# Kernel tuning notes

Hardware: AMD Instinct MI355X
Metric: run time of the kernel (lower is better)

Reference implementation:

```python
import jax, jax.numpy as jnp
import numpy as np

D_MODEL = 1024
NUM_HEADS = 16
HEAD_DIM = D_MODEL // NUM_HEADS


def setup_inputs() -> dict:
    key = jax.random.key(0)
    ks = jax.random.split(key, 9)
    s = D_MODEL ** -0.5  # roughly like nn.Linear init scale
    x = jax.random.normal(ks[0], (4, 2048, D_MODEL), dtype=jnp.float32)
    Wq = jax.random.normal(ks[1], (D_MODEL, D_MODEL), dtype=jnp.float32) * s
    bq = jax.random.normal(ks[2], (D_MODEL,), dtype=jnp.float32) * s
    Wk = jax.random.normal(ks[3], (D_MODEL, D_MODEL), dtype=jnp.float32) * s
    bk = jax.random.normal(ks[4], (D_MODEL,), dtype=jnp.float32) * s
    Wv = jax.random.normal(ks[5], (D_MODEL, D_MODEL), dtype=jnp.float32) * s
    bv = jax.random.normal(ks[6], (D_MODEL,), dtype=jnp.float32) * s
    Wo = jax.random.normal(ks[7], (D_MODEL, D_MODEL), dtype=jnp.float32) * s
    bo = jax.random.normal(ks[8], (D_MODEL,), dtype=jnp.float32) * s
    return {"x": x, "Wq": Wq, "bq": bq, "Wk": Wk, "bk": bk,
            "Wv": Wv, "bv": bv, "Wo": Wo, "bo": bo}


def reference(x, Wq, bq, Wk, bk, Wv, bv, Wo, bo):
    B, S, D = x.shape
    H, Dh = NUM_HEADS, HEAD_DIM
    scale = Dh ** -0.5
    # nn.Linear: x @ W.T + b
    q = (x @ Wq.T + bq).reshape(B, S, H, Dh)
    k = (x @ Wk.T + bk).reshape(B, S, H, Dh)
    v = (x @ Wv.T + bv).reshape(B, S, H, Dh)
    # scores: (B, H, S, S), full materialization as in the original bmm path
    dp = scale * jnp.einsum('bqhd,bkhd->bhqk', q, k)
    att = jax.nn.softmax(dp, axis=-1)
    out = jnp.einsum('bhqk,bkhd->bqhd', att, v).reshape(B, S, D)
    return out @ Wo.T + bo
```

## Files before the change

kernel.cpp:

```cpp
#include <hip/hip_runtime.h>
#include <stdint.h>

typedef __attribute__((ext_vector_type(8))) __bf16 bf16x8;
typedef __attribute__((ext_vector_type(4))) float floatx4;

#define DEV __device__ __forceinline__

DEV unsigned short f2bf(float f) {
    union { float f; unsigned u; } uf; uf.f = f;
    unsigned u = uf.u;
    unsigned r = (u + 0x7fffu + ((u >> 16) & 1u)) >> 16;
    return (unsigned short)r;
}

DEV float fast_exp2(float x) {
#if __has_builtin(__builtin_amdgcn_exp2f)
    return __builtin_amdgcn_exp2f(x);
#else
    return exp2f(x);
#endif
}

DEV unsigned pack_trunc2(float lo, float hi) {
    return __builtin_amdgcn_perm(__float_as_uint(hi), __float_as_uint(lo), 0x07060302u);
}

DEV void async16(const void* g, void* l) {
    __builtin_amdgcn_global_load_lds(
        (const __attribute__((address_space(1))) void*)g,
        (__attribute__((address_space(3))) void*)l, 16, 0, 0);
}

__global__ void cast_all_kernel(const float* __restrict__ x,
                                const float* __restrict__ Wq, const float* __restrict__ Wk,
                                const float* __restrict__ Wv, const float* __restrict__ Wo,
                                const float* __restrict__ bq, const float* __restrict__ bk,
                                const float* __restrict__ bv,
                                unsigned short* __restrict__ xb,
                                unsigned short* __restrict__ wqkv,
                                unsigned short* __restrict__ wo,
                                float* __restrict__ bqkv) {
    const int NX = 2097152;
    const int NW = 262144;
    int i = blockIdx.x * blockDim.x + threadIdx.x;
    if (i < NX) {
        float4 v = reinterpret_cast<const float4*>(x)[i];
        ushort4 o;
        o.x = f2bf(v.x); o.y = f2bf(v.y); o.z = f2bf(v.z); o.w = f2bf(v.w);
        reinterpret_cast<ushort4*>(xb)[i] = o;
        return;
    }
    int j = i - NX;
    if (j < 4 * NW) {
        int seg = j >> 18, off = j & (NW - 1);
        const float* src = (seg == 0) ? Wq : (seg == 1) ? Wk : (seg == 2) ? Wv : Wo;
        unsigned short* dst = (seg < 3) ? (wqkv + seg * 1048576) : wo;
        float4 v = reinterpret_cast<const float4*>(src)[off];
        ushort4 o;
        o.x = f2bf(v.x); o.y = f2bf(v.y); o.z = f2bf(v.z); o.w = f2bf(v.w);
        reinterpret_cast<ushort4*>(dst)[off] = o;
        return;
    }
    int k = j - 4 * NW;
    if (k < 768) {
        int seg = k >> 8, off = k & 255;
        const float* src = (seg == 0) ? bq : (seg == 1) ? bk : bv;
        reinterpret_cast<float4*>(bqkv)[k] = reinterpret_cast<const float4*>(src)[off];
    }
}

template <int MODE>
__global__ __launch_bounds__(256)
void gemm128(const unsigned short* __restrict__ A,
             const unsigned short* __restrict__ B,
             const float* __restrict__ bias,
             unsigned short* __restrict__ q_ws,
             unsigned short* __restrict__ k_ws,
             unsigned short* __restrict__ v_ws,
             float* __restrict__ fout) {
    constexpr int K = 1024;
    __shared__ alignas(16) unsigned short smem[128 * 136];
    unsigned short* sA = smem;
    unsigned short* sB = smem + 128 * 64;
    unsigned short* sT = smem;
    float* sT32 = reinterpret_cast<float*>(smem);

    const int tid = threadIdx.x;
    const int w = tid >> 6, lane = tid & 63, quad = lane >> 4, l16 = lane & 15;
    const int wr = w >> 1, wc = w & 1;
    const int bm = blockIdx.x, bn = blockIdx.y;
    const int arow0 = bm * 128, brow0 = bn * 128;

    floatx4 acc[4][4];
#pragma unroll
    for (int i = 0; i < 4; i++)
#pragma unroll
        for (int j = 0; j < 4; j++) acc[i][j] = (floatx4){0.f, 0.f, 0.f, 0.f};

    for (int k0 = 0; k0 < K; k0 += 64) {
#pragma unroll
        for (int i = 0; i < 4; i++) {
            int cb = i * 256 + w * 64;
            int ci = cb + lane;
            int row = ci >> 3, cl = ci & 7, cs = cl ^ (row & 7);
            async16(A + (size_t)(arow0 + row) * K + k0 + cs * 8, (char*)sA + cb * 16);
            async16(B + (size_t)(brow0 + row) * K + k0 + cs * 8, (char*)sB + cb * 16);
        }
        __syncthreads();
#pragma unroll
        for (int kk = 0; kk < 2; kk++) {
            bf16x8 aF[4], bF[4];
#pragma unroll
            for (int i = 0; i < 4; i++) {
                int row = wr * 64 + i * 16 + l16;
                int c = kk * 4 + quad, ph = c ^ (row & 7);
                aF[i] = *reinterpret_cast<const bf16x8*>(sA + row * 64 + ph * 8);
            }
#pragma unroll
            for (int j = 0; j < 4; j++) {
                int row = wc * 64 + j * 16 + l16;
                int c = kk * 4 + quad, ph = c ^ (row & 7);
                bF[j] = *reinterpret_cast<const bf16x8*>(sB + row * 64 + ph * 8);
            }
#pragma unroll
            for (int i = 0; i < 4; i++)
#pragma unroll
                for (int j = 0; j < 4; j++)
                    acc[i][j] = __builtin_amdgcn_mfma_f32_16x16x32_bf16(
                        aF[i], bF[j], acc[i][j], 0, 0, 0);
        }
        __syncthreads();
    }

    if (MODE == 1) {
#pragma unroll
        for (int ch = 0; ch < 2; ch++) {
            if (ch) __syncthreads();
            if (wr == ch) {
#pragma unroll
                for (int j = 0; j < 4; j++) {
                    const int c = wc * 64 + j * 16 + l16;
                    const float bia = bias[brow0 + c];
#pragma unroll
                    for (int i = 0; i < 4; i++) {
                        int s_loc = i * 16 + quad * 4;
#pragma unroll
                        for (int r = 0; r < 4; r++)
                            sT32[(s_loc + r) * 132 + c] = acc[i][j][r] + bia;
                    }
                }
            }
            __syncthreads();
            const int cpos = (tid & 31) * 4;
#pragma unroll
            for (int it = 0; it < 8; it++) {
                int s_loc = (tid >> 5) + it * 8;
                int grow = arow0 + ch * 64 + s_loc;
                float4 vv = *reinterpret_cast<const float4*>(sT32 + s_loc * 132 + cpos);
                *reinterpret_cast<float4*>(fout + (size_t)grow * 1024 + brow0 + cpos) = vv;
            }
        }
    } else if (bn < 16) {
        unsigned short* dst = (bn < 8) ? q_ws : k_ws;
        const float sc = (bn < 8) ? 0.18033688f : 1.0f;
#pragma unroll
        for (int j = 0; j < 4; j++) {
            const int c = wc * 64 + j * 16 + l16;
            const float bia = bias[brow0 + c];
#pragma unroll
            for (int i = 0; i < 4; i++) {
                int s_loc = wr * 64 + i * 16 + quad * 4;
#pragma unroll
                for (int r = 0; r < 4; r++)
                    sT[(s_loc + r) * 136 + c] = f2bf((acc[i][j][r] + bia) * sc);
            }
        }
        __syncthreads();
        const int nnbase = (bn & 7) * 128;
        const int c0 = (tid & 15) * 8;
        const int h = (nnbase + c0) >> 6, d = c0 & 63;
#pragma unroll
        for (int it = 0; it < 8; it++) {
            int s_loc = (tid >> 4) + it * 16;
            int s = arow0 + s_loc;
            int bb = s >> 11, s4 = s & 2047;
            uint4 vdat = *reinterpret_cast<const uint4*>(sT + s_loc * 136 + c0);
            *reinterpret_cast<uint4*>(
                dst + ((size_t)(bb * 16 + h) * 2048 + s4) * 64 + d) = vdat;
        }
    } else {
#pragma unroll
        for (int j = 0; j < 4; j++) {
            const int c = wc * 64 + j * 16 + l16;
            const float bia = bias[brow0 + c];
#pragma unroll
            for (int i = 0; i < 4; i++) {
#pragma unroll
                for (int r = 0; r < 4; r++) {
                    int v = wr * 64 + (quad * 4 + r) * 4 + i;
                    sT[c * 136 + v] = f2bf(acc[i][j][r] + bia);
                }
            }
        }
        __syncthreads();
        const int bb = bm >> 4, blk = bm & 15;
        const int chunk = tid & 15;
#pragma unroll
        for (int it = 0; it < 8; it++) {
            int row = (tid >> 4) + it * 16;
            int h = (bn - 16) * 2 + (row >> 6), d = row & 63;
            ushort4 lo = *reinterpret_cast<const ushort4*>(sT + row * 136 + chunk * 8);
            ushort4 hi = *reinterpret_cast<const ushort4*>(sT + row * 136 + chunk * 8 + 4);
            size_t off = ((size_t)(bb * 16 + h) * 64 + d) * 2048 + blk * 128 + chunk * 8;
            *reinterpret_cast<ushort4*>(v_ws + off) = lo;
            *reinterpret_cast<ushort4*>(v_ws + off + 4) = hi;
        }
    }
}

__global__ __launch_bounds__(256, 4)
void attn_kernel(const unsigned short* __restrict__ q_ws,
                 const unsigned short* __restrict__ k_ws,
                 const unsigned short* __restrict__ v_ws,
                 unsigned short* __restrict__ o_ws) {
    __shared__ alignas(16) unsigned short smem[20480];

    const int tid = threadIdx.x;
    const int w = tid >> 6, lane = tid & 63, quad = lane >> 4, l16 = lane & 15;
    const int id = blockIdx.x;
    const int bh = (id >> 7) * 8 + (id & 7);
    const int q0 = ((id >> 3) & 15) * 128;
    const size_t base = (size_t)bh * 2048 * 64;

    unsigned short* sPw = smem + 16384 + w * 1024;

    bf16x8 aQ[2][2];
#pragma unroll
    for (int g = 0; g < 2; g++) {
        int qrow = q0 + g * 64 + w * 16 + l16;
        const unsigned short* qp = q_ws + base + (size_t)qrow * 64 + quad * 8;
        aQ[g][0] = *reinterpret_cast<const bf16x8*>(qp);
        aQ[g][1] = *reinterpret_cast<const bf16x8*>(qp + 32);
    }

    const unsigned short* kg[2];
    const unsigned short* vg[2];
    int loff[2];
#pragma unroll
    for (int it = 0; it < 2; it++) {
        int ci = it * 256 + tid;
        int row = ci >> 3, cl = ci & 7, cs = cl ^ (row & 7);
        kg[it] = k_ws + base + (size_t)row * 64 + cs * 8;
        vg[it] = v_ws + base + (size_t)row * 2048 + cs * 8;
        loff[it] = ci * 8;
    }

    const __bf16 one = (__bf16)1.0f;
    const bf16x8 vOnes = {one, one, one, one, one, one, one, one};

    floatx4 oAcc[2][4], rsAcc[2];
#pragma unroll
    for (int g = 0; g < 2; g++) {
#pragma unroll
        for (int j = 0; j < 4; j++) oAcc[g][j] = (floatx4){0.f, 0.f, 0.f, 0.f};
        rsAcc[g] = (floatx4){0.f, 0.f, 0.f, 0.f};
    }

    {
#pragma unroll
        for (int it = 0; it < 2; it++) {
            async16(kg[it], smem + loff[it]);
            async16(vg[it], smem + 8192 + loff[it]);
        }
    }

    for (int t = 0; t < 32; t++) {
        const int b = t & 1;
        const unsigned short* sK = smem + b * 4096;
        const unsigned short* sVt = smem + 8192 + b * 4096;
        __syncthreads();

        if (t < 31) {
            const int kv0 = (t + 1) * 64;
            unsigned short* dK = smem + (b ^ 1) * 4096;
            unsigned short* dV = smem + 8192 + (b ^ 1) * 4096;
#pragma unroll
            for (int it = 0; it < 2; it++) {
                async16(kg[it] + (size_t)kv0 * 64, dK + loff[it]);
                async16(vg[it] + kv0, dV + loff[it]);
            }
        }

#pragma unroll
        for (int g = 0; g < 2; g++) {
            floatx4 sAcc[4];
#pragma unroll
            for (int j = 0; j < 4; j++) sAcc[j] = (floatx4){0.f, 0.f, 0.f, 0.f};
#pragma unroll
            for (int kk = 0; kk < 2; kk++) {
#pragma unroll
                for (int j = 0; j < 4; j++) {
                    int krow = j * 16 + l16;
                    int ph = (kk * 4 + quad) ^ (krow & 7);
                    bf16x8 aK = *reinterpret_cast<const bf16x8*>(sK + krow * 64 + ph * 8);
                    sAcc[j] = __builtin_amdgcn_mfma_f32_16x16x32_bf16(
                        aK, aQ[g][kk], sAcc[j], 0, 0, 0);
                }
            }

            {
                float e00 = fast_exp2(sAcc[0][0]), e10 = fast_exp2(sAcc[1][0]);
                float e20 = fast_exp2(sAcc[2][0]), e30 = fast_exp2(sAcc[3][0]);
                float e01 = fast_exp2(sAcc[0][1]), e11 = fast_exp2(sAcc[1][1]);
                float e21 = fast_exp2(sAcc[2][1]), e31 = fast_exp2(sAcc[3][1]);
                float e02 = fast_exp2(sAcc[0][2]), e12 = fast_exp2(sAcc[1][2]);
                float e22 = fast_exp2(sAcc[2][2]), e32 = fast_exp2(sAcc[3][2]);
                float e03 = fast_exp2(sAcc[0][3]), e13 = fast_exp2(sAcc[1][3]);
                float e23 = fast_exp2(sAcc[2][3]), e33 = fast_exp2(sAcc[3][3]);
                uint4 w0, w1;
                w0.x = pack_trunc2(e00, e10);
                w0.y = pack_trunc2(e20, e30);
                w0.z = pack_trunc2(e01, e11);
                w0.w = pack_trunc2(e21, e31);
                w1.x = pack_trunc2(e02, e12);
                w1.y = pack_trunc2(e22, e32);
                w1.z = pack_trunc2(e03, e13);
                w1.w = pack_trunc2(e23, e33);
                const int xr = l16 & 7;
                *reinterpret_cast<uint4*>(sPw + l16 * 64 + (((2 * quad) ^ xr) << 3)) = w0;
                *reinterpret_cast<uint4*>(sPw + l16 * 64 + (((2 * quad + 1) ^ xr) << 3)) = w1;
            }
            asm volatile("s_waitcnt lgkmcnt(0)" ::: "memory");
            __builtin_amdgcn_sched_barrier(0);

            bf16x8 aP[2];
#pragma unroll
            for (int ks = 0; ks < 2; ks++)
                aP[ks] = *reinterpret_cast<const bf16x8*>(
                    sPw + l16 * 64 + (((ks * 4 + quad) ^ (l16 & 7)) << 3));
#pragma unroll
            for (int jd = 0; jd < 4; jd++) {
                int drow = jd * 16 + l16;
#pragma unroll
                for (int ks = 0; ks < 2; ks++) {
                    int ph = (ks * 4 + quad) ^ (drow & 7);
                    bf16x8 bV = *reinterpret_cast<const bf16x8*>(sVt + drow * 64 + ph * 8);
                    oAcc[g][jd] = __builtin_amdgcn_mfma_f32_16x16x32_bf16(
                        aP[ks], bV, oAcc[g][jd], 0, 0, 0);
                }
            }
#pragma unroll
            for (int ks = 0; ks < 2; ks++)
                rsAcc[g] = __builtin_amdgcn_mfma_f32_16x16x32_bf16(
                    aP[ks], vOnes, rsAcc[g], 0, 0, 0);
        }
    }

    const int bb = bh >> 4, h = bh & 15;
#pragma unroll
    for (int g = 0; g < 2; g++) {
        float inv[4];
#pragma unroll
        for (int r = 0; r < 4; r++) inv[r] = 1.0f / rsAcc[g][r];
#pragma unroll
        for (int jd = 0; jd < 4; jd++) {
            int d = jd * 16 + l16;
#pragma unroll
            for (int r = 0; r < 4; r++) {
                int s = q0 + g * 64 + w * 16 + quad * 4 + r;
                float v = oAcc[g][jd][r] * inv[r];
                o_ws[((size_t)bb * 2048 + s) * 1024 + h * 64 + d] = f2bf(v);
            }
        }
    }
}

extern "C" void kernel_launch(void* const* d_in, const int* in_sizes, int n_in,
                              void* d_out, int out_size, void* d_ws, size_t ws_size,
                              hipStream_t stream) {
    const float* x  = (const float*)d_in[0];
    const float* Wq = (const float*)d_in[1];
    const float* bq = (const float*)d_in[2];
    const float* Wk = (const float*)d_in[3];
    const float* bk = (const float*)d_in[4];
    const float* Wv = (const float*)d_in[5];
    const float* bv = (const float*)d_in[6];
    const float* Wo = (const float*)d_in[7];
    const float* bo = (const float*)d_in[8];
    float* out = (float*)d_out;

    char* ws = (char*)d_ws;
    unsigned short* xb   = (unsigned short*)(ws);
    unsigned short* wqkv = (unsigned short*)(ws + (16ull << 20));
    unsigned short* wo   = (unsigned short*)(ws + (22ull << 20));
    float*          bqkv = (float*)(ws + (24ull << 20));
    unsigned short* q_ws = (unsigned short*)(ws + (25ull << 20));
    unsigned short* k_ws = (unsigned short*)(ws + (41ull << 20));
    unsigned short* v_ws = (unsigned short*)(ws + (57ull << 20));
    unsigned short* o_ws = xb;

    cast_all_kernel<<<12291, 256, 0, stream>>>(x, Wq, Wk, Wv, Wo, bq, bk, bv,
                                               xb, wqkv, wo, bqkv);

    gemm128<0><<<dim3(64, 24), 256, 0, stream>>>(xb, wqkv, bqkv, q_ws, k_ws, v_ws, nullptr);
    attn_kernel<<<1024, 256, 0, stream>>>(q_ws, k_ws, v_ws, o_ws);
    gemm128<1><<<dim3(64, 8), 256, 0, stream>>>(o_ws, wo, bo, nullptr, nullptr, nullptr, out);
}
```

Measured before the change: 275.9 us.

## Interleave two query groups in attention loop and retile output projection GEMM

The attention inner loop now computes QK^T for both 64-row query groups together, sharing each K fragment load between the two groups. The exp2 and pack of the second group are interleaved with the PV MFMAs of the first, so MFMA and VALU work can overlap. Separately, the output projection moves to a dedicated 128x64-tile GEMM launched on a 64x16 grid, doubling block count to fill more CUs. The cost is higher register pressure from holding two score sets, plus more A-tile reloads in the projection.

```diff
diff --git a/kernel.cpp b/kernel.cpp
--- a/kernel.cpp
+++ b/kernel.cpp
@@ -83,7 +83,6 @@
     unsigned short* sA = smem;
     unsigned short* sB = smem + 128 * 64;
     unsigned short* sT = smem;
-    float* sT32 = reinterpret_cast<float*>(smem);
 
     const int tid = threadIdx.x;
     const int w = tid >> 6, lane = tid & 63, quad = lane >> 4, l16 = lane & 15;
@@ -132,35 +131,7 @@
         __syncthreads();
     }
 
-    if (MODE == 1) {
-#pragma unroll
-        for (int ch = 0; ch < 2; ch++) {
-            if (ch) __syncthreads();
-            if (wr == ch) {
-#pragma unroll
-                for (int j = 0; j < 4; j++) {
-                    const int c = wc * 64 + j * 16 + l16;
-                    const float bia = bias[brow0 + c];
-#pragma unroll
-                    for (int i = 0; i < 4; i++) {
-                        int s_loc = i * 16 + quad * 4;
-#pragma unroll
-                        for (int r = 0; r < 4; r++)
-                            sT32[(s_loc + r) * 132 + c] = acc[i][j][r] + bia;
-                    }
-                }
-            }
-            __syncthreads();
-            const int cpos = (tid & 31) * 4;
-#pragma unroll
-            for (int it = 0; it < 8; it++) {
-                int s_loc = (tid >> 5) + it * 8;
-                int grow = arow0 + ch * 64 + s_loc;
-                float4 vv = *reinterpret_cast<const float4*>(sT32 + s_loc * 132 + cpos);
-                *reinterpret_cast<float4*>(fout + (size_t)grow * 1024 + brow0 + cpos) = vv;
-            }
-        }
-    } else if (bn < 16) {
+    if (bn < 16) {
         unsigned short* dst = (bn < 8) ? q_ws : k_ws;
         const float sc = (bn < 8) ? 0.18033688f : 1.0f;
 #pragma unroll
@@ -218,6 +189,97 @@
     }
 }
 
+__global__ __launch_bounds__(256)
+void gemm_oproj(const unsigned short* __restrict__ A,
+                const unsigned short* __restrict__ Bw,
+                const float* __restrict__ bias,
+                float* __restrict__ fout) {
+    constexpr int K = 1024;
+    __shared__ alignas(16) unsigned short smem[192 * 64];
+    unsigned short* sA = smem;
+    unsigned short* sB = smem + 128 * 64;
+    float* sT32 = reinterpret_cast<float*>(smem);
+
+    const int tid = threadIdx.x;
+    const int w = tid >> 6, lane = tid & 63, quad = lane >> 4, l16 = lane & 15;
+    const int wr = w >> 1, wc = w & 1;
+    const int bm = blockIdx.x, bn = blockIdx.y;
+    const int arow0 = bm * 128, brow0 = bn * 64;
+
+    floatx4 acc[4][2];
+#pragma unroll
+    for (int i = 0; i < 4; i++)
+#pragma unroll
+        for (int j = 0; j < 2; j++) acc[i][j] = (floatx4){0.f, 0.f, 0.f, 0.f};
+
+    for (int k0 = 0; k0 < K; k0 += 64) {
+#pragma unroll
+        for (int i = 0; i < 4; i++) {
+            int ci = i * 256 + tid;
+            int row = ci >> 3, cs = (ci & 7) ^ (row & 7);
+            async16(A + (size_t)(arow0 + row) * K + k0 + cs * 8, (char*)sA + ci * 16);
+        }
+#pragma unroll
+        for (int i = 0; i < 2; i++) {
+            int ci = i * 256 + tid;
+            int row = ci >> 3, cs = (ci & 7) ^ (row & 7);
+            async16(Bw + (size_t)(brow0 + row) * K + k0 + cs * 8, (char*)sB + ci * 16);
+        }
+        __syncthreads();
+#pragma unroll
+        for (int kk = 0; kk < 2; kk++) {
+            bf16x8 aF[4], bF[2];
+#pragma unroll
+            for (int i = 0; i < 4; i++) {
+                int row = wr * 64 + i * 16 + l16;
+                int ph = (kk * 4 + quad) ^ (row & 7);
+                aF[i] = *reinterpret_cast<const bf16x8*>(sA + row * 64 + ph * 8);
+            }
+#pragma unroll
+            for (int j = 0; j < 2; j++) {
+                int row = wc * 32 + j * 16 + l16;
+                int ph = (kk * 4 + quad) ^ (row & 7);
+                bF[j] = *reinterpret_cast<const bf16x8*>(sB + row * 64 + ph * 8);
+            }
+#pragma unroll
+            for (int i = 0; i < 4; i++)
+#pragma unroll
+                for (int j = 0; j < 2; j++)
+                    acc[i][j] = __builtin_amdgcn_mfma_f32_16x16x32_bf16(
+                        aF[i], bF[j], acc[i][j], 0, 0, 0);
+        }
+        __syncthreads();
+    }
+
+#pragma unroll
+    for (int ch = 0; ch < 2; ch++) {
+        if (ch) __syncthreads();
+        if (wr == ch) {
+#pragma unroll
+            for (int j = 0; j < 2; j++) {
+                const int c = wc * 32 + j * 16 + l16;
+                const float bia = bias[brow0 + c];
+#pragma unroll
+                for (int i = 0; i < 4; i++) {
+                    int s_loc = i * 16 + quad * 4;
+#pragma unroll
+                    for (int r = 0; r < 4; r++)
+                        sT32[(s_loc + r) * 68 + c] = acc[i][j][r] + bia;
+                }
+            }
+        }
+        __syncthreads();
+        const int cpos = (tid & 15) * 4;
+#pragma unroll
+        for (int it = 0; it < 4; it++) {
+            int s_loc = (tid >> 4) + it * 16;
+            int grow = arow0 + ch * 64 + s_loc;
+            float4 vv = *reinterpret_cast<const float4*>(sT32 + s_loc * 68 + cpos);
+            *reinterpret_cast<float4*>(fout + (size_t)grow * 1024 + brow0 + cpos) = vv;
+        }
+    }
+}
+
 __global__ __launch_bounds__(256, 4)
 void attn_kernel(const unsigned short* __restrict__ q_ws,
                  const unsigned short* __restrict__ k_ws,
@@ -274,6 +336,12 @@
         }
     }
 
+    const int xr = l16 & 7;
+    const int offw0 = l16 * 64 + (((2 * quad) ^ xr) << 3);
+    const int offw1 = l16 * 64 + (((2 * quad + 1) ^ xr) << 3);
+    const int offr0 = l16 * 64 + ((quad ^ xr) << 3);
+    const int offr1 = l16 * 64 + (((4 + quad) ^ xr) << 3);
+
     for (int t = 0; t < 32; t++) {
         const int b = t & 1;
         const unsigned short* sK = smem + b * 4096;
@@ -291,68 +359,99 @@
             }
         }
 
-#pragma unroll
-        for (int g = 0; g < 2; g++) {
-            floatx4 sAcc[4];
-#pragma unroll
-            for (int j = 0; j < 4; j++) sAcc[j] = (floatx4){0.f, 0.f, 0.f, 0.f};
-#pragma unroll
-            for (int kk = 0; kk < 2; kk++) {
-#pragma unroll
-                for (int j = 0; j < 4; j++) {
-                    int krow = j * 16 + l16;
-                    int ph = (kk * 4 + quad) ^ (krow & 7);
-                    bf16x8 aK = *reinterpret_cast<const bf16x8*>(sK + krow * 64 + ph * 8);
-                    sAcc[j] = __builtin_amdgcn_mfma_f32_16x16x32_bf16(
-                        aK, aQ[g][kk], sAcc[j], 0, 0, 0);
-                }
-            }
-
-            {
-                float e00 = fast_exp2(sAcc[0][0]), e10 = fast_exp2(sAcc[1][0]);
-                float e20 = fast_exp2(sAcc[2][0]), e30 = fast_exp2(sAcc[3][0]);
-                float e01 = fast_exp2(sAcc[0][1]), e11 = fast_exp2(sAcc[1][1]);
-                float e21 = fast_exp2(sAcc[2][1]), e31 = fast_exp2(sAcc[3][1]);
-                float e02 = fast_exp2(sAcc[0][2]), e12 = fast_exp2(sAcc[1][2]);
-                float e22 = fast_exp2(sAcc[2][2]), e32 = fast_exp2(sAcc[3][2]);
-                float e03 = fast_exp2(sAcc[0][3]), e13 = fast_exp2(sAcc[1][3]);
-                float e23 = fast_exp2(sAcc[2][3]), e33 = fast_exp2(sAcc[3][3]);
-                uint4 w0, w1;
-                w0.x = pack_trunc2(e00, e10);
-                w0.y = pack_trunc2(e20, e30);
-                w0.z = pack_trunc2(e01, e11);
-                w0.w = pack_trunc2(e21, e31);
-                w1.x = pack_trunc2(e02, e12);
-                w1.y = pack_trunc2(e22, e32);
-                w1.z = pack_trunc2(e03, e13);
-                w1.w = pack_trunc2(e23, e33);
-                const int xr = l16 & 7;
-                *reinterpret_cast<uint4*>(sPw + l16 * 64 + (((2 * quad) ^ xr) << 3)) = w0;
-                *reinterpret_cast<uint4*>(sPw + l16 * 64 + (((2 * quad + 1) ^ xr) << 3)) = w1;
-            }
-            asm volatile("s_waitcnt lgkmcnt(0)" ::: "memory");
-            __builtin_amdgcn_sched_barrier(0);
-
-            bf16x8 aP[2];
-#pragma unroll
-            for (int ks = 0; ks < 2; ks++)
-                aP[ks] = *reinterpret_cast<const bf16x8*>(
-                    sPw + l16 * 64 + (((ks * 4 + quad) ^ (l16 & 7)) << 3));
+        floatx4 s0[4], s1[4];
+#pragma unroll
+        for (int j = 0; j < 4; j++) {
+            s0[j] = (floatx4){0.f, 0.f, 0.f, 0.f};
+            s1[j] = (floatx4){0.f, 0.f, 0.f, 0.f};
+        }
+#pragma unroll
+        for (int kk = 0; kk < 2; kk++) {
+#pragma unroll
+            for (int j = 0; j < 4; j++) {
+                int krow = j * 16 + l16;
+                int ph = (kk * 4 + quad) ^ (krow & 7);
+                bf16x8 aK = *reinterpret_cast<const bf16x8*>(sK + krow * 64 + ph * 8);
+                s0[j] = __builtin_amdgcn_mfma_f32_16x16x32_bf16(aK, aQ[0][kk], s0[j], 0, 0, 0);
+                s1[j] = __builtin_amdgcn_mfma_f32_16x16x32_bf16(aK, aQ[1][kk], s1[j], 0, 0, 0);
+            }
+        }
+
+#pragma unroll
+        for (int j = 0; j < 4; j++)
+#pragma unroll
+            for (int r = 0; r < 4; r++) s0[j][r] = fast_exp2(s0[j][r]);
+        {
+            uint4 w0, w1;
+            w0.x = pack_trunc2(s0[0][0], s0[1][0]);
+            w0.y = pack_trunc2(s0[2][0], s0[3][0]);
+            w0.z = pack_trunc2(s0[0][1], s0[1][1]);
+            w0.w = pack_trunc2(s0[2][1], s0[3][1]);
+            w1.x = pack_trunc2(s0[0][2], s0[1][2]);
+            w1.y = pack_trunc2(s0[2][2], s0[3][2]);
+            w1.z = pack_trunc2(s0[0][3], s0[1][3]);
+            w1.w = pack_trunc2(s0[2][3], s0[3][3]);
+            *reinterpret_cast<uint4*>(sPw + offw0) = w0;
+            *reinterpret_cast<uint4*>(sPw + offw1) = w1;
+        }
+
+#pragma unroll
+        for (int j = 0; j < 4; j++)
+#pragma unroll
+            for (int r = 0; r < 4; r++) s1[j][r] = fast_exp2(s1[j][r]);
+
+        asm volatile("s_waitcnt lgkmcnt(0)" ::: "memory");
+        __builtin_amdgcn_sched_barrier(0);
+
+        {
+            bf16x8 aPa = *reinterpret_cast<const bf16x8*>(sPw + offr0);
+            bf16x8 aPb = *reinterpret_cast<const bf16x8*>(sPw + offr1);
 #pragma unroll
             for (int jd = 0; jd < 4; jd++) {
                 int drow = jd * 16 + l16;
-#pragma unroll
-                for (int ks = 0; ks < 2; ks++) {
-                    int ph = (ks * 4 + quad) ^ (drow & 7);
-                    bf16x8 bV = *reinterpret_cast<const bf16x8*>(sVt + drow * 64 + ph * 8);
-                    oAcc[g][jd] = __builtin_amdgcn_mfma_f32_16x16x32_bf16(
-                        aP[ks], bV, oAcc[g][jd], 0, 0, 0);
-                }
-            }
-#pragma unroll
-            for (int ks = 0; ks < 2; ks++)
-                rsAcc[g] = __builtin_amdgcn_mfma_f32_16x16x32_bf16(
-                    aP[ks], vOnes, rsAcc[g], 0, 0, 0);
+                int ph0 = quad ^ (drow & 7);
+                bf16x8 bVa = *reinterpret_cast<const bf16x8*>(sVt + drow * 64 + ph0 * 8);
+                oAcc[0][jd] = __builtin_amdgcn_mfma_f32_16x16x32_bf16(aPa, bVa, oAcc[0][jd], 0, 0, 0);
+                int ph1 = (4 + quad) ^ (drow & 7);
+                bf16x8 bVb = *reinterpret_cast<const bf16x8*>(sVt + drow * 64 + ph1 * 8);
+                oAcc[0][jd] = __builtin_amdgcn_mfma_f32_16x16x32_bf16(aPb, bVb, oAcc[0][jd], 0, 0, 0);
+            }
+            rsAcc[0] = __builtin_amdgcn_mfma_f32_16x16x32_bf16(aPa, vOnes, rsAcc[0], 0, 0, 0);
+            rsAcc[0] = __builtin_amdgcn_mfma_f32_16x16x32_bf16(aPb, vOnes, rsAcc[0], 0, 0, 0);
+        }
+
+        {
+            uint4 w0, w1;
+            w0.x = pack_trunc2(s1[0][0], s1[1][0]);
+            w0.y = pack_trunc2(s1[2][0], s1[3][0]);
+            w0.z = pack_trunc2(s1[0][1], s1[1][1]);
+            w0.w = pack_trunc2(s1[2][1], s1[3][1]);
+            w1.x = pack_trunc2(s1[0][2], s1[1][2]);
+            w1.y = pack_trunc2(s1[2][2], s1[3][2]);
+            w1.z = pack_trunc2(s1[0][3], s1[1][3]);
+            w1.w = pack_trunc2(s1[2][3], s1[3][3]);
+            *reinterpret_cast<uint4*>(sPw + offw0) = w0;
+            *reinterpret_cast<uint4*>(sPw + offw1) = w1;
+        }
+
+        asm volatile("s_waitcnt lgkmcnt(0)" ::: "memory");
+        __builtin_amdgcn_sched_barrier(0);
+
+        {
+            bf16x8 aPa = *reinterpret_cast<const bf16x8*>(sPw + offr0);
+            bf16x8 aPb = *reinterpret_cast<const bf16x8*>(sPw + offr1);
+#pragma unroll
+            for (int jd = 0; jd < 4; jd++) {
+                int drow = jd * 16 + l16;
+                int ph0 = quad ^ (drow & 7);
+                bf16x8 bVa = *reinterpret_cast<const bf16x8*>(sVt + drow * 64 + ph0 * 8);
+                oAcc[1][jd] = __builtin_amdgcn_mfma_f32_16x16x32_bf16(aPa, bVa, oAcc[1][jd], 0, 0, 0);
+                int ph1 = (4 + quad) ^ (drow & 7);
+                bf16x8 bVb = *reinterpret_cast<const bf16x8*>(sVt + drow * 64 + ph1 * 8);
+                oAcc[1][jd] = __builtin_amdgcn_mfma_f32_16x16x32_bf16(aPb, bVb, oAcc[1][jd], 0, 0, 0);
+            }
+            rsAcc[1] = __builtin_amdgcn_mfma_f32_16x16x32_bf16(aPa, vOnes, rsAcc[1], 0, 0, 0);
+            rsAcc[1] = __builtin_amdgcn_mfma_f32_16x16x32_bf16(aPb, vOnes, rsAcc[1], 0, 0, 0);
         }
     }
 
@@ -404,5 +503,5 @@
 
     gemm128<0><<<dim3(64, 24), 256, 0, stream>>>(xb, wqkv, bqkv, q_ws, k_ws, v_ws, nullptr);
     attn_kernel<<<1024, 256, 0, stream>>>(q_ws, k_ws, v_ws, o_ws);
-    gemm128<1><<<dim3(64, 8), 256, 0, stream>>>(o_ws, wo, bo, nullptr, nullptr, nullptr, out);
-}
+    gemm_oproj<<<dim3(64, 16), 256, 0, stream>>>(o_ws, wo, bo, out);
+}
```

Measured after the change: 266.5 us. -3.4%, faster.
